# Kernel tuning notes

Hardware: AMD Instinct MI355X
Metric: run time of the kernel (lower is better)

## Reference

```python
import jax, jax.numpy as jnp
import numpy as np

K = 3  # involution kernel size


def dwconv3x3(x, w, b):
    # x: [B,C,H,W], w: [C,1,3,3] (depthwise, groups=C), b: [C]
    y = jax.lax.conv_general_dilated(
        x, w, window_strides=(1, 1), padding='SAME',
        dimension_numbers=('NCHW', 'OIHW', 'NCHW'),
        feature_group_count=x.shape[1])
    return y + b[None, :, None, None]


def conv1x1(x, w, b):
    # x: [B,C,H,W], w: [O,C], b: [O]
    return jnp.einsum('oc,bchw->bohw', w, x) + b[None, :, None, None]


def extract_patches(x):
    # x: [B,C,H,W] -> [B,C,K*K,H,W], zero-padded 'same' 3x3 neighborhoods
    B, C, H, W = x.shape
    p = (K - 1) // 2
    xp = jnp.pad(x, ((0, 0), (0, 0), (p, p), (p, p)))
    return jnp.stack([xp[:, :, i:i + H, j:j + W]
                      for i in range(K) for j in range(K)], axis=2)


def involution(x, w_red, b_red, w_span, b_span):
    # dynamic per-pixel kernels: [B, K*K, H, W]
    kern = conv1x1(jax.nn.relu(conv1x1(x, w_red, b_red)), w_span, b_span)
    patches = extract_patches(x)                 # [B,C,KK,H,W]
    return jnp.einsum('bkhw,bckhw->bchw', kern, patches)


def setup_inputs() -> dict:
    key = jax.random.key(0)
    ks = jax.random.split(key, 10)
    dim, red = 256, 64  # reduction ratio 4
    B, H, W = 8, 64, 64
    s = 0.05
    return {
        'x': jax.random.normal(ks[0], (B, dim, H, W), jnp.float32),
        'w_in': jax.random.normal(ks[1], (dim, 1, 3, 3), jnp.float32) * s,
        'b_in': jax.random.normal(ks[2], (dim,), jnp.float32) * s,
        'w_red': jax.random.normal(ks[3], (red, dim), jnp.float32) * s,
        'b_red': jax.random.normal(ks[4], (red,), jnp.float32) * s,
        'w_span': jax.random.normal(ks[5], (K * K, red), jnp.float32) * s,
        'b_span': jax.random.normal(ks[6], (K * K,), jnp.float32) * s,
        'w_out': jax.random.normal(ks[7], (dim, 1, 3, 3), jnp.float32) * s,
        'b_out': jax.random.normal(ks[8], (dim,), jnp.float32) * s,
    }


def reference(x, w_in, b_in, w_red, b_red, w_span, b_span, w_out, b_out):
    x = dwconv3x3(x, w_in, b_in)
    x = involution(x, w_red, b_red, w_span, b_span)
    x = dwconv3x3(x, w_out, b_out)
    return x
```

## Files before the change

kernel.cpp:

```cpp
#include <hip/hip_runtime.h>

#define BB 8
#define CC 256
#define HH 64
#define WW 64
#define RED 64
#define HW 4096
#define AST 72
#define LSF 68
#define LSH 72

typedef __attribute__((ext_vector_type(8))) short s8v;
typedef __attribute__((ext_vector_type(4))) float f4v;

__device__ __forceinline__ unsigned short f2bf(float f) {
    unsigned u = __float_as_uint(f);
    u += 0x7fff + ((u >> 16) & 1);
    return (unsigned short)(u >> 16);
}
__device__ __forceinline__ float b2f(unsigned short u) {
    return __uint_as_float(((unsigned)u) << 16);
}

__global__ __launch_bounds__(512, 4) void dw_kern(const float* __restrict__ x,
                                                  const float* __restrict__ w_in,
                                                  const float* __restrict__ b_in,
                                                  const float* __restrict__ w_red,
                                                  const float* __restrict__ b_red,
                                                  const float* __restrict__ w_span,
                                                  const float* __restrict__ b_span,
                                                  float* __restrict__ kern,
                                                  unsigned short* __restrict__ x1g) {
    alignas(16) __shared__ char smem[16640 + 18432];
    unsigned short* xs = (unsigned short*)smem;
    float* r_lds = (float*)smem;
    float* part  = (float*)(smem + 16640);

    const int t  = threadIdx.x;
    const int bx = blockIdx.x;
    const int h  = ((bx & 7) << 3) | (bx >> 3);
    const int b  = blockIdx.y;
    const int l  = t & 63;
    const int wv = t >> 6;
    const int mt = wv & 3, nh = wv >> 2;
    const int m0 = mt << 4;
    const int q  = t & 15;
    const int w0 = q << 2;
    const int cr = t >> 4;

    float4 pv[2][3]; float plf[2][3], prt[2][3];

    auto loadX = [&](int c0) {
        #pragma unroll
        for (int s = 0; s < 2; s++) {
            const int cc = c0 + s * 32 + cr;
            const float* xp = x + ((size_t)(b * CC + cc)) * HW;
            #pragma unroll
            for (int ky = 0; ky < 3; ky++) {
                int hh = h + ky - 1;
                if (hh < 0 || hh >= HH) {
                    pv[s][ky] = make_float4(0.f, 0.f, 0.f, 0.f);
                    plf[s][ky] = 0.f; prt[s][ky] = 0.f;
                    continue;
                }
                const float* row = xp + hh * WW + w0;
                pv[s][ky]  = *(const float4*)row;
                plf[s][ky] = (w0 > 0)      ? row[-1] : 0.f;
                prt[s][ky] = (w0 + 4 < WW) ? row[4]  : 0.f;
            }
        }
    };
    auto computeA = [&](int c0) {
        #pragma unroll
        for (int s = 0; s < 2; s++) {
            const int cl = s * 32 + cr;
            const int cc = c0 + cl;
            const float* wp = w_in + cc * 9;
            const float bb = b_in[cc];
            float4 a4 = make_float4(bb, bb, bb, bb);
            #pragma unroll
            for (int ky = 0; ky < 3; ky++) {
                float4 v = pv[s][ky];
                float lf = plf[s][ky], rt = prt[s][ky];
                float k0 = wp[ky * 3 + 0], k1 = wp[ky * 3 + 1], k2 = wp[ky * 3 + 2];
                a4.x = fmaf(k0, lf,  a4.x); a4.y = fmaf(k0, v.x, a4.y);
                a4.z = fmaf(k0, v.y, a4.z); a4.w = fmaf(k0, v.z, a4.w);
                a4.x = fmaf(k1, v.x, a4.x); a4.y = fmaf(k1, v.y, a4.y);
                a4.z = fmaf(k1, v.z, a4.z); a4.w = fmaf(k1, v.w, a4.w);
                a4.x = fmaf(k2, v.y, a4.x); a4.y = fmaf(k2, v.z, a4.y);
                a4.z = fmaf(k2, v.w, a4.z); a4.w = fmaf(k2, rt,  a4.w);
            }
            ushort4 pk;
            pk.x = f2bf(a4.x); pk.y = f2bf(a4.y);
            pk.z = f2bf(a4.z); pk.w = f2bf(a4.w);
            xs[(w0 + 0) * AST + cl] = pk.x;
            xs[(w0 + 1) * AST + cl] = pk.y;
            xs[(w0 + 2) * AST + cl] = pk.z;
            xs[(w0 + 3) * AST + cl] = pk.w;
            *(ushort4*)(x1g + ((size_t)(b * CC + cc)) * HW + h * WW + w0) = pk;
        }
    };

    s8v bfr[2][2];
    auto loadB = [&](int k) {
        #pragma unroll
        for (int kb = 0; kb < 2; kb++)
            #pragma unroll
            for (int ntl = 0; ntl < 2; ntl++) {
                const int o   = (((nh << 1) + ntl) << 4) + (l & 15);
                const int c0b = (((k << 1) + kb) << 5) + ((l >> 4) & 3) * 8;
                const float* wr = w_red + o * CC + c0b;
                float4 f0 = *(const float4*)wr;
                float4 f1 = *(const float4*)(wr + 4);
                s8v bv;
                bv[0] = (short)f2bf(f0.x); bv[1] = (short)f2bf(f0.y);
                bv[2] = (short)f2bf(f0.z); bv[3] = (short)f2bf(f0.w);
                bv[4] = (short)f2bf(f1.x); bv[5] = (short)f2bf(f1.y);
                bv[6] = (short)f2bf(f1.z); bv[7] = (short)f2bf(f1.w);
                bfr[kb][ntl] = bv;
            }
    };

    f4v acc[2] = {{0.f, 0.f, 0.f, 0.f}, {0.f, 0.f, 0.f, 0.f}};

    loadX(0); loadB(0);
    for (int k = 0; k < 4; k++) {
        computeA(k << 6);
        if (k < 3) loadX((k + 1) << 6);
        __syncthreads();
        #pragma unroll
        for (int kb = 0; kb < 2; kb++) {
            const unsigned short* ap =
                xs + (m0 + (l & 15)) * AST + (kb << 5) + ((l >> 4) & 3) * 8;
            s8v av = *(const s8v*)ap;
            #pragma unroll
            for (int ntl = 0; ntl < 2; ntl++)
                acc[ntl] = __builtin_amdgcn_mfma_f32_16x16x32_bf16(
                    av, bfr[kb][ntl], acc[ntl], 0, 0, 0);
        }
        if (k < 3) loadB(k + 1);
        __syncthreads();
    }

    #pragma unroll
    for (int ntl = 0; ntl < 2; ntl++) {
        int o = ((nh << 1) + ntl) * 16 + (l & 15);
        int pxr = m0 + ((l >> 4) & 3) * 4;
        #pragma unroll
        for (int i = 0; i < 4; i++)
            r_lds[o * 65 + pxr + i] = acc[ntl][i];
    }
    __syncthreads();

    const int px = t & 63;
    const int o0 = __builtin_amdgcn_readfirstlane(wv << 3);
    float kk[9];
    #pragma unroll
    for (int j = 0; j < 9; j++) kk[j] = 0.f;
    #pragma unroll
    for (int i = 0; i < 8; i++) {
        float r = fmaxf(r_lds[(o0 + i) * 65 + px] + b_red[o0 + i], 0.f);
        #pragma unroll
        for (int j = 0; j < 9; j++) kk[j] = fmaf(w_span[j * RED + o0 + i], r, kk[j]);
    }
    #pragma unroll
    for (int j = 0; j < 9; j++) part[(wv * 9 + j) * 64 + px] = kk[j];
    __syncthreads();
    if (wv == 0) {
        float* kp = kern + (size_t)b * 9 * HW + h * WW + px;
        #pragma unroll
        for (int j = 0; j < 9; j++) {
            float s = b_span[j];
            #pragma unroll
            for (int g = 0; g < 8; g++) s += part[(g * 9 + j) * 64 + px];
            kp[j * HW] = s;
        }
    }
}

__global__ __launch_bounds__(256) void invol_dw(const unsigned short* __restrict__ x1g,
                                                const float* __restrict__ kern,
                                                const float* __restrict__ w_out,
                                                const float* __restrict__ b_out,
                                                float* __restrict__ out) {
    __shared__ unsigned short x1s[HH * LSH];
    __shared__ float res[HH * LSF];
    const int t  = threadIdx.x;
    const int q  = t & 15;
    const int w0 = q << 2;
    const int r  = t >> 4;
    const int c = blockIdx.x, b = blockIdx.y;

    {
        const unsigned short* xp = x1g + ((size_t)(b * CC + c)) * HW;
        const int hl = t >> 2;
        const int wl = (t & 3) << 4;
        *(s8v*)&x1s[hl * LSH + wl]     = *(const s8v*)(xp + hl * WW + wl);
        *(s8v*)&x1s[hl * LSH + wl + 8] = *(const s8v*)(xp + hl * WW + wl + 8);
    }
    __syncthreads();

    const float* kp = kern + (size_t)b * 9 * HW;
    #pragma unroll
    for (int i = 0; i < 4; i++) {
        int h  = r + (i << 4);
        int hw = h * WW + w0;
        float4 acc = make_float4(0.f, 0.f, 0.f, 0.f);
        #pragma unroll
        for (int ky = 0; ky < 3; ky++) {
            int hh = h + ky - 1;
            if (hh < 0 || hh >= HH) continue;
            const unsigned short* row = &x1s[hh * LSH + w0];
            float vx = b2f(row[0]), vy = b2f(row[1]);
            float vz = b2f(row[2]), vw = b2f(row[3]);
            float lf = (w0 > 0)      ? b2f(row[-1]) : 0.f;
            float rt = (w0 + 4 < WW) ? b2f(row[4])  : 0.f;
            float4 k0 = *(const float4*)(kp + (ky * 3 + 0) * HW + hw);
            float4 k1 = *(const float4*)(kp + (ky * 3 + 1) * HW + hw);
            float4 k2 = *(const float4*)(kp + (ky * 3 + 2) * HW + hw);
            acc.x = fmaf(k0.x, lf, acc.x); acc.y = fmaf(k0.y, vx, acc.y);
            acc.z = fmaf(k0.z, vy, acc.z); acc.w = fmaf(k0.w, vz, acc.w);
            acc.x = fmaf(k1.x, vx, acc.x); acc.y = fmaf(k1.y, vy, acc.y);
            acc.z = fmaf(k1.z, vz, acc.z); acc.w = fmaf(k1.w, vw, acc.w);
            acc.x = fmaf(k2.x, vy, acc.x); acc.y = fmaf(k2.y, vz, acc.y);
            acc.z = fmaf(k2.z, vw, acc.z); acc.w = fmaf(k2.w, rt, acc.w);
        }
        *(float4*)&res[h * LSF + w0] = acc;
    }
    __syncthreads();

    const float* wp = w_out + c * 9;
    const float bb = b_out[c];
    float* op = out + ((size_t)(b * CC + c)) * HW;
    #pragma unroll
    for (int i = 0; i < 4; i++) {
        int h = r + (i << 4);
        float4 acc = make_float4(bb, bb, bb, bb);
        #pragma unroll
        for (int ky = 0; ky < 3; ky++) {
            int hh = h + ky - 1;
            if (hh < 0 || hh >= HH) continue;
            const float* row = &res[hh * LSF + w0];
            float4 v = *(const float4*)row;
            float lf = (w0 > 0)      ? row[-1] : 0.f;
            float rt = (w0 + 4 < WW) ? row[4]  : 0.f;
            float k0 = wp[ky * 3 + 0], k1 = wp[ky * 3 + 1], k2 = wp[ky * 3 + 2];
            acc.x = fmaf(k0, lf,  acc.x); acc.y = fmaf(k0, v.x, acc.y);
            acc.z = fmaf(k0, v.y, acc.z); acc.w = fmaf(k0, v.z, acc.w);
            acc.x = fmaf(k1, v.x, acc.x); acc.y = fmaf(k1, v.y, acc.y);
            acc.z = fmaf(k1, v.z, acc.z); acc.w = fmaf(k1, v.w, acc.w);
            acc.x = fmaf(k2, v.y, acc.x); acc.y = fmaf(k2, v.z, acc.y);
            acc.z = fmaf(k2, v.w, acc.z); acc.w = fmaf(k2, rt,  acc.w);
        }
        *(float4*)(op + h * WW + w0) = acc;
    }
}

extern "C" void kernel_launch(void* const* d_in, const int* in_sizes, int n_in,
                              void* d_out, int out_size, void* d_ws, size_t ws_size,
                              hipStream_t stream) {
    const float* x      = (const float*)d_in[0];
    const float* w_in   = (const float*)d_in[1];
    const float* b_in   = (const float*)d_in[2];
    const float* w_red  = (const float*)d_in[3];
    const float* b_red  = (const float*)d_in[4];
    const float* w_span = (const float*)d_in[5];
    const float* b_span = (const float*)d_in[6];
    const float* w_out  = (const float*)d_in[7];
    const float* b_out  = (const float*)d_in[8];
    float* out = (float*)d_out;

    float* kern = (float*)d_ws;
    unsigned short* x1g = (unsigned short*)(kern + (size_t)BB * 9 * HW);

    dw_kern<<<dim3(HH, BB), 512, 0, stream>>>(x, w_in, b_in, w_red, b_red,
                                              w_span, b_span, kern, x1g);
    invol_dw<<<dim3(CC, BB), 256, 0, stream>>>(x1g, kern, w_out, b_out, out);
}
```

Measured before the change: 155.6 us.

## Split dw_kern rows into half-width blocks and prepack bf16 reduction weights

The first kernel now has each block handle half a row (32 pixels) with 256 threads, doubling the grid to 128x8 blocks. The MFMA tiling and the final reduction are adjusted to match. A new small kernel converts w_red to bf16 once, already laid out in MFMA fragment order, so each block loads B operands with a single vector load instead of converting fp32 values inline. The depthwise weights and bias are staged in LDS as well. This aims for better occupancy and less per-block conversion work, at the cost of an extra launch and duplicate halo/weight loads across the two half-row blocks.

```diff
diff --git a/kernel.cpp b/kernel.cpp
--- a/kernel.cpp
+++ b/kernel.cpp
@@ -22,31 +22,52 @@
     return __uint_as_float(((unsigned)u) << 16);
 }
 
-__global__ __launch_bounds__(512, 4) void dw_kern(const float* __restrict__ x,
+__global__ __launch_bounds__(256) void build_wtf(const float* __restrict__ w_red,
+                                                 unsigned short* __restrict__ wtf) {
+    int e = blockIdx.x * 256 + threadIdx.x;
+    int j = e & 7, l = (e >> 3) & 63, nt = (e >> 9) & 3, kbg = e >> 11;
+    int o = nt * 16 + (l & 15);
+    int c = kbg * 32 + ((l >> 4) & 3) * 8 + j;
+    wtf[e] = f2bf(w_red[o * CC + c]);
+}
+
+__global__ __launch_bounds__(256, 4) void dw_kern(const float* __restrict__ x,
                                                   const float* __restrict__ w_in,
                                                   const float* __restrict__ b_in,
-                                                  const float* __restrict__ w_red,
+                                                  const unsigned short* __restrict__ wtf,
                                                   const float* __restrict__ b_red,
                                                   const float* __restrict__ w_span,
                                                   const float* __restrict__ b_span,
                                                   float* __restrict__ kern,
                                                   unsigned short* __restrict__ x1g) {
-    alignas(16) __shared__ char smem[16640 + 18432];
+    alignas(16) __shared__ char smem[8448 + 12288];
     unsigned short* xs = (unsigned short*)smem;
     float* r_lds = (float*)smem;
-    float* part  = (float*)(smem + 16640);
-
-    const int t  = threadIdx.x;
-    const int bx = blockIdx.x;
-    const int h  = ((bx & 7) << 3) | (bx >> 3);
-    const int b  = blockIdx.y;
+    float* wl    = (float*)(smem + 8448);
+    float* part  = (float*)(smem + 8448);
+
+    const int t    = threadIdx.x;
+    const int bx   = blockIdx.x;
+    const int band = bx & 7;
+    const int idx  = bx >> 3;
+    const int h    = band * 8 + (idx >> 1);
+    const int wh   = idx & 1;
+    const int b    = blockIdx.y;
     const int l  = t & 63;
     const int wv = t >> 6;
-    const int mt = wv & 3, nh = wv >> 2;
+    const int mt = wv & 1, nh = wv >> 1;
     const int m0 = mt << 4;
-    const int q  = t & 15;
-    const int w0 = q << 2;
-    const int cr = t >> 4;
+    const int q  = t & 7;
+    const int pl = q << 2;
+    const int wg = (wh << 5) | pl;
+    const int cr = t >> 3;
+
+    #pragma unroll
+    for (int j = 0; j < 9; j++) {
+        int i = j * 256 + t;
+        wl[(i / 9) * 12 + (i % 9)] = w_in[i];
+    }
+    wl[t * 12 + 9] = b_in[t];
 
     float4 pv[2][3]; float plf[2][3], prt[2][3];
 
@@ -63,10 +84,10 @@
                     plf[s][ky] = 0.f; prt[s][ky] = 0.f;
                     continue;
                 }
-                const float* row = xp + hh * WW + w0;
+                const float* row = xp + hh * WW + wg;
                 pv[s][ky]  = *(const float4*)row;
-                plf[s][ky] = (w0 > 0)      ? row[-1] : 0.f;
-                prt[s][ky] = (w0 + 4 < WW) ? row[4]  : 0.f;
+                plf[s][ky] = (wg > 0)      ? row[-1] : 0.f;
+                prt[s][ky] = (wg + 4 < WW) ? row[4]  : 0.f;
             }
         }
     };
@@ -75,14 +96,17 @@
         for (int s = 0; s < 2; s++) {
             const int cl = s * 32 + cr;
             const int cc = c0 + cl;
-            const float* wp = w_in + cc * 9;
-            const float bb = b_in[cc];
-            float4 a4 = make_float4(bb, bb, bb, bb);
+            const float* wp = wl + cc * 12;
+            float4 wa = *(const float4*)wp;
+            float4 wb = *(const float4*)(wp + 4);
+            float2 wc = *(const float2*)(wp + 8);
+            float4 a4 = make_float4(wc.y, wc.y, wc.y, wc.y);
+            const float kw[9] = {wa.x, wa.y, wa.z, wa.w, wb.x, wb.y, wb.z, wb.w, wc.x};
             #pragma unroll
             for (int ky = 0; ky < 3; ky++) {
                 float4 v = pv[s][ky];
                 float lf = plf[s][ky], rt = prt[s][ky];
-                float k0 = wp[ky * 3 + 0], k1 = wp[ky * 3 + 1], k2 = wp[ky * 3 + 2];
+                float k0 = kw[ky * 3 + 0], k1 = kw[ky * 3 + 1], k2 = kw[ky * 3 + 2];
                 a4.x = fmaf(k0, lf,  a4.x); a4.y = fmaf(k0, v.x, a4.y);
                 a4.z = fmaf(k0, v.y, a4.z); a4.w = fmaf(k0, v.z, a4.w);
                 a4.x = fmaf(k1, v.x, a4.x); a4.y = fmaf(k1, v.y, a4.y);
@@ -93,11 +117,11 @@
             ushort4 pk;
             pk.x = f2bf(a4.x); pk.y = f2bf(a4.y);
             pk.z = f2bf(a4.z); pk.w = f2bf(a4.w);
-            xs[(w0 + 0) * AST + cl] = pk.x;
-            xs[(w0 + 1) * AST + cl] = pk.y;
-            xs[(w0 + 2) * AST + cl] = pk.z;
-            xs[(w0 + 3) * AST + cl] = pk.w;
-            *(ushort4*)(x1g + ((size_t)(b * CC + cc)) * HW + h * WW + w0) = pk;
+            xs[(pl + 0) * AST + cl] = pk.x;
+            xs[(pl + 1) * AST + cl] = pk.y;
+            xs[(pl + 2) * AST + cl] = pk.z;
+            xs[(pl + 3) * AST + cl] = pk.w;
+            *(ushort4*)(x1g + ((size_t)(b * CC + cc)) * HW + h * WW + wg) = pk;
         }
     };
 
@@ -107,23 +131,16 @@
         for (int kb = 0; kb < 2; kb++)
             #pragma unroll
             for (int ntl = 0; ntl < 2; ntl++) {
-                const int o   = (((nh << 1) + ntl) << 4) + (l & 15);
-                const int c0b = (((k << 1) + kb) << 5) + ((l >> 4) & 3) * 8;
-                const float* wr = w_red + o * CC + c0b;
-                float4 f0 = *(const float4*)wr;
-                float4 f1 = *(const float4*)(wr + 4);
-                s8v bv;
-                bv[0] = (short)f2bf(f0.x); bv[1] = (short)f2bf(f0.y);
-                bv[2] = (short)f2bf(f0.z); bv[3] = (short)f2bf(f0.w);
-                bv[4] = (short)f2bf(f1.x); bv[5] = (short)f2bf(f1.y);
-                bv[6] = (short)f2bf(f1.z); bv[7] = (short)f2bf(f1.w);
-                bfr[kb][ntl] = bv;
+                int nt = (nh << 1) + ntl;
+                int kbg = (k << 1) + kb;
+                bfr[kb][ntl] = *(const s8v*)(wtf + (((kbg * 4 + nt) * 64 + l) << 3));
             }
     };
 
     f4v acc[2] = {{0.f, 0.f, 0.f, 0.f}, {0.f, 0.f, 0.f, 0.f}};
 
     loadX(0); loadB(0);
+    __syncthreads();
     for (int k = 0; k < 4; k++) {
         computeA(k << 6);
         if (k < 3) loadX((k + 1) << 6);
@@ -148,33 +165,40 @@
         int pxr = m0 + ((l >> 4) & 3) * 4;
         #pragma unroll
         for (int i = 0; i < 4; i++)
-            r_lds[o * 65 + pxr + i] = acc[ntl][i];
-    }
-    __syncthreads();
-
-    const int px = t & 63;
-    const int o0 = __builtin_amdgcn_readfirstlane(wv << 3);
+            r_lds[o * 33 + pxr + i] = acc[ntl][i];
+    }
+    __syncthreads();
+
+    const int px = t & 31;
+    const int og = t >> 5;
+    const int o0 = og << 3;
     float kk[9];
     #pragma unroll
     for (int j = 0; j < 9; j++) kk[j] = 0.f;
     #pragma unroll
     for (int i = 0; i < 8; i++) {
-        float r = fmaxf(r_lds[(o0 + i) * 65 + px] + b_red[o0 + i], 0.f);
+        float r = fmaxf(r_lds[(o0 + i) * 33 + px] + b_red[o0 + i], 0.f);
         #pragma unroll
         for (int j = 0; j < 9; j++) kk[j] = fmaf(w_span[j * RED + o0 + i], r, kk[j]);
     }
-    #pragma unroll
-    for (int j = 0; j < 9; j++) part[(wv * 9 + j) * 64 + px] = kk[j];
-    __syncthreads();
-    if (wv == 0) {
-        float* kp = kern + (size_t)b * 9 * HW + h * WW + px;
-        #pragma unroll
-        for (int j = 0; j < 9; j++) {
-            float s = b_span[j];
-            #pragma unroll
-            for (int g = 0; g < 8; g++) s += part[(g * 9 + j) * 64 + px];
-            kp[j * HW] = s;
-        }
+    __syncthreads();
+    #pragma unroll
+    for (int j = 0; j < 9; j++) part[(og * 9 + j) * 32 + px] = kk[j];
+    __syncthreads();
+
+    float* kp = kern + (size_t)b * 9 * HW + h * WW + (wh << 5) + px;
+    const int jj = t >> 5;
+    {
+        float s = b_span[jj];
+        #pragma unroll
+        for (int g = 0; g < 8; g++) s += part[(g * 9 + jj) * 32 + px];
+        kp[jj * HW] = s;
+    }
+    if (t < 32) {
+        float s = b_span[8];
+        #pragma unroll
+        for (int g = 0; g < 8; g++) s += part[(g * 9 + 8) * 32 + px];
+        kp[8 * HW] = s;
     }
 }
 
@@ -194,9 +218,9 @@
     {
         const unsigned short* xp = x1g + ((size_t)(b * CC + c)) * HW;
         const int hl = t >> 2;
-        const int wl = (t & 3) << 4;
-        *(s8v*)&x1s[hl * LSH + wl]     = *(const s8v*)(xp + hl * WW + wl);
-        *(s8v*)&x1s[hl * LSH + wl + 8] = *(const s8v*)(xp + hl * WW + wl + 8);
+        const int wl2 = (t & 3) << 4;
+        *(s8v*)&x1s[hl * LSH + wl2]     = *(const s8v*)(xp + hl * WW + wl2);
+        *(s8v*)&x1s[hl * LSH + wl2 + 8] = *(const s8v*)(xp + hl * WW + wl2 + 8);
     }
     __syncthreads();
 
@@ -272,8 +296,10 @@
 
     float* kern = (float*)d_ws;
     unsigned short* x1g = (unsigned short*)(kern + (size_t)BB * 9 * HW);
-
-    dw_kern<<<dim3(HH, BB), 512, 0, stream>>>(x, w_in, b_in, w_red, b_red,
-                                              w_span, b_span, kern, x1g);
+    unsigned short* wtf = x1g + (size_t)BB * CC * HW;
+
+    build_wtf<<<64, 256, 0, stream>>>(w_red, wtf);
+    dw_kern<<<dim3(128, BB), 256, 0, stream>>>(x, w_in, b_in, wtf, b_red,
+                                               w_span, b_span, kern, x1g);
     invol_dw<<<dim3(CC, BB), 256, 0, stream>>>(x1g, kern, w_out, b_out, out);
 }
```

Result: faster. 138.1 us (-11.2%).
